# Optimization experiments

Measured on AMD Instinct MI355X. Metric: run time of the kernel, lower is better.

## Reference

```python
import jax, jax.numpy as jnp
import numpy as np

N, D, E = 50000, 128, 800000


def setup_inputs() -> dict:
    key = jax.random.key(0)
    ks = jax.random.split(key, 12)
    s = 1.0 / np.sqrt(D)
    return {
        "x": jax.random.normal(ks[0], (N, D), jnp.float32),
        "edge_index": jax.random.randint(ks[1], (2, E), 0, N, jnp.int32),
        "W1": jax.random.normal(ks[2], (D, D), jnp.float32) * s,
        "bc1": jnp.zeros((D,), jnp.float32),
        "W2": jax.random.normal(ks[3], (D, D), jnp.float32) * s,
        "bc2": jnp.zeros((D,), jnp.float32),
        "w11": jax.random.normal(ks[4], (D, D), jnp.float32) * s,
        "w12": jax.random.normal(ks[5], (D, D), jnp.float32) * s,
        "b1": jax.random.uniform(ks[6], (D,), jnp.float32, -s, s),
        "w21": jax.random.normal(ks[7], (D, D), jnp.float32) * s,
        "w22": jax.random.normal(ks[8], (D, D), jnp.float32) * s,
        "b2": jax.random.uniform(ks[9], (D,), jnp.float32, -s, s),
    }


def gcn_conv(x, W, b, src, dst):
    """PyG GCNConv: self-loops + symmetric D^-1/2 (A+I) D^-1/2 normalization."""
    n = x.shape[0]
    h = x @ W  # [N, D]
    ones = jnp.ones(dst.shape[0], h.dtype)
    deg = jax.ops.segment_sum(ones, dst, num_segments=n) + 1.0  # +1 for self-loop
    dinv = jax.lax.rsqrt(deg)
    norm = dinv[src] * dinv[dst]  # [E]
    agg = jax.ops.segment_sum(h[src] * norm[:, None], dst, num_segments=n)
    agg = agg + h * (dinv * dinv)[:, None]  # self-loop messages
    return agg + b


def reference(x, edge_index, W1, bc1, W2, bc2, w11, w12, b1, w21, w22, b2):
    src, dst = edge_index[0], edge_index[1]
    # layer 1: forward and reversed edge directions (dropout is identity in eval)
    o1 = jax.nn.relu(gcn_conv(x, W1, bc1, src, dst))
    o2 = jax.nn.relu(gcn_conv(x, W1, bc1, dst, src))
    G = jax.nn.sigmoid(o1 @ w11.T + o2 @ w12.T + b1)
    h = G * o1 + (1.0 - G) * o2
    # layer 2
    p1 = jax.nn.relu(gcn_conv(h, W2, bc2, src, dst))
    p2 = jax.nn.relu(gcn_conv(h, W2, bc2, dst, src))
    G2 = jax.nn.sigmoid(p1 @ w21.T + p2 @ w22.T + b2)
    return G2 * p1 + (1.0 - G2) * p2
```

## Files before the change

### kernel.cpp

```cpp
#include <hip/hip_runtime.h>
#include <hip/hip_bf16.h>
#include <hip/hip_fp16.h>
#include <math.h>

#define D 128
#define SEG 4096
#define BSH 7
#define RCAP 4096
#define ACAP 4096

typedef _Float16 half8  __attribute__((ext_vector_type(8)));
typedef _Float16 half4v __attribute__((ext_vector_type(4)));
typedef float    fx4    __attribute__((ext_vector_type(4)));

__global__ __launch_bounds__(256) void scat2_kernel(const int* __restrict__ src,
                                                    const int* __restrict__ dst,
                                                    int e, int nb,
                                                    int* __restrict__ gcur1, int* __restrict__ gcur2,
                                                    unsigned int* __restrict__ rec1,
                                                    unsigned int* __restrict__ rec2) {
    __shared__ int h1[512], h2[512], o1[512], o2[512], run1[512], run2[512];
    int tid = threadIdx.x;
    for (int b = tid; b < nb; b += 256) { h1[b] = 0; h2[b] = 0; run1[b] = 0; run2[b] = 0; }
    __syncthreads();
    int s0 = blockIdx.x * SEG;
    int s1 = min(e, s0 + SEG);
    for (int idx = s0 + tid; idx < s1; idx += 256) {
        atomicAdd(&h1[dst[idx] >> BSH], 1);
        atomicAdd(&h2[src[idx] >> BSH], 1);
    }
    __syncthreads();
    for (int b = tid; b < nb; b += 256) {
        o1[b] = atomicAdd(&gcur1[b], h1[b]);
        o2[b] = atomicAdd(&gcur2[b], h2[b]);
    }
    __syncthreads();
    for (int idx = s0 + tid; idx < s1; idx += 256) {
        unsigned int sv = (unsigned int)src[idx];
        unsigned int dv = (unsigned int)dst[idx];
        int b1 = dv >> BSH, b2 = sv >> BSH;
        int p1 = o1[b1] + atomicAdd(&run1[b1], 1);
        if (p1 < RCAP) rec1[(size_t)b1 * RCAP + p1] = (dv << 16) | sv;
        int p2 = o2[b2] + atomicAdd(&run2[b2], 1);
        if (p2 < RCAP) rec2[(size_t)b2 * RCAP + p2] = (sv << 16) | dv;
    }
}

__global__ __launch_bounds__(256) void fin_kernel(const unsigned int* __restrict__ rec1,
                                                  const unsigned int* __restrict__ rec2,
                                                  const int* __restrict__ gcur1, const int* __restrict__ gcur2,
                                                  unsigned short* __restrict__ adj1, unsigned short* __restrict__ adj2,
                                                  int* __restrict__ ip1, int* __restrict__ ipe1,
                                                  int* __restrict__ ip2, int* __restrict__ ipe2,
                                                  float* __restrict__ dinv1, float* __restrict__ dinv2,
                                                  int n) {
    __shared__ unsigned int Lrec[RCAP];
    __shared__ unsigned short sadj[ACAP];
    __shared__ int deg[128], pscan[128], cur[128];
    __shared__ int ptot_s;
    int bkt = blockIdx.x;
    int dir = blockIdx.y;
    const unsigned int* rec = dir ? rec2 : rec1;
    const int* gc = dir ? gcur2 : gcur1;
    unsigned short* adj = dir ? adj2 : adj1;
    int* ip  = dir ? ip2 : ip1;
    int* ipe = dir ? ipe2 : ipe1;
    float* dinv = dir ? dinv2 : dinv1;

    int tid = threadIdx.x;
    int cnt = gc[bkt];
    if (cnt > RCAP) cnt = RCAP;
    size_t rbase = (size_t)bkt * RCAP;
    if (tid < 128) { deg[tid] = 0; cur[tid] = 0; }
    for (int i = tid; i < cnt; i += 256) Lrec[i] = rec[rbase + i];
    __syncthreads();
    int base = bkt << BSH;
    for (int i = tid; i < cnt; i += 256)
        atomicAdd(&deg[(int)(Lrec[i] >> 16) - base], 1);
    __syncthreads();
    if (tid < 128) pscan[tid] = (deg[tid] + 7) & ~7;
    __syncthreads();
    #pragma unroll
    for (int st = 1; st < 128; st <<= 1) {
        int add = (tid < 128 && tid >= st) ? pscan[tid - st] : 0;
        __syncthreads();
        if (tid < 128) pscan[tid] += add;
        __syncthreads();
    }
    if (tid == 127) ptot_s = min(pscan[127], ACAP);
    __syncthreads();
    int ptot = ptot_s;
    for (int i = tid; i < ptot; i += 256) sadj[i] = (unsigned short)n;
    __syncthreads();
    for (int i = tid; i < cnt; i += 256) {
        unsigned int r = Lrec[i];
        int l = (int)(r >> 16) - base;
        int pd = (deg[l] + 7) & ~7;
        int pos = pscan[l] - pd + atomicAdd(&cur[l], 1);
        if (pos < ACAP) sadj[pos] = (unsigned short)(r & 0xffffu);
    }
    __syncthreads();
    int gbase = bkt * ACAP;
    for (int i = tid; i < ptot; i += 256) adj[gbase + i] = sadj[i];
    if (tid < 128) {
        int node = base + tid;
        if (node < n) {
            int pd = (deg[tid] + 7) & ~7;
            ip[node]  = gbase + pscan[tid] - pd;
            ipe[node] = gbase + pscan[tid];
            dinv[node] = rsqrtf((float)deg[tid] + 1.0f);
        }
    }
    if (bkt == 0 && tid == 200) dinv[n] = 0.0f;
}

__global__ __launch_bounds__(256) void transwh_kernel(const float* __restrict__ W1, const float* __restrict__ W2,
                                                      _Float16* __restrict__ T1, _Float16* __restrict__ T2) {
    __shared__ float s[32][33];
    const float* w = blockIdx.y ? W2 : W1;
    _Float16* t = blockIdx.y ? T2 : T1;
    int tk = (blockIdx.x >> 2) * 32;
    int tc = (blockIdx.x & 3) * 32;
    int lr = threadIdx.x >> 5;
    int lc = threadIdx.x & 31;
    #pragma unroll
    for (int i = 0; i < 32; i += 8)
        s[lr + i][lc] = w[(size_t)(tk + lr + i) * D + tc + lc];
    __syncthreads();
    #pragma unroll
    for (int i = 0; i < 32; i += 8)
        t[(size_t)(tc + lr + i) * D + tk + lc] = (_Float16)s[lc][lr + i];
}

__global__ __launch_bounds__(256) void convh_kernel(const float* __restrict__ w11, const float* __restrict__ w12,
                                                    const float* __restrict__ w21, const float* __restrict__ w22,
                                                    _Float16* __restrict__ o11, _Float16* __restrict__ o12,
                                                    _Float16* __restrict__ o21, _Float16* __restrict__ o22) {
    const float* w = (blockIdx.y == 0) ? w11 : (blockIdx.y == 1) ? w12 : (blockIdx.y == 2) ? w21 : w22;
    _Float16* o = (blockIdx.y == 0) ? o11 : (blockIdx.y == 1) ? o12 : (blockIdx.y == 2) ? o21 : o22;
    int idx = (blockIdx.x * 256 + threadIdx.x) * 4;
    float4 v = *(const float4*)&w[idx];
    half4v h = {(_Float16)v.x, (_Float16)v.y, (_Float16)v.z, (_Float16)v.w};
    *(half4v*)&o[idx] = h;
}

__global__ __launch_bounds__(256) void gemm_f32a_kernel(const float* __restrict__ A,
                                                        const _Float16* __restrict__ Wt,
                                                        _Float16* __restrict__ C16, int n) {
    int tid = threadIdx.x;
    int wv = tid >> 6, lane = tid & 63;
    int m = lane & 15, q = lane >> 4;
    int row0 = blockIdx.x * 128 + wv * 32;
    size_t ar0 = (size_t)min(row0 + m, n - 1) * D;
    size_t ar1 = (size_t)min(row0 + 16 + m, n - 1) * D;
    fx4 acc[2][8];
    #pragma unroll
    for (int t = 0; t < 2; t++)
        #pragma unroll
        for (int ct = 0; ct < 8; ct++) acc[t][ct] = (fx4){0.f, 0.f, 0.f, 0.f};
    #pragma unroll
    for (int ks = 0; ks < 4; ks++) {
        int k0 = ks * 32 + q * 8;
        half8 bf[8];
        #pragma unroll
        for (int ct = 0; ct < 8; ct++)
            bf[ct] = *(const half8*)&Wt[(size_t)(ct * 16 + m) * D + k0];
        float4 u0 = *(const float4*)&A[ar0 + k0];
        float4 u1 = *(const float4*)&A[ar0 + k0 + 4];
        half8 a0 = {(_Float16)u0.x, (_Float16)u0.y, (_Float16)u0.z, (_Float16)u0.w,
                    (_Float16)u1.x, (_Float16)u1.y, (_Float16)u1.z, (_Float16)u1.w};
        float4 v0 = *(const float4*)&A[ar1 + k0];
        float4 v1 = *(const float4*)&A[ar1 + k0 + 4];
        half8 a1 = {(_Float16)v0.x, (_Float16)v0.y, (_Float16)v0.z, (_Float16)v0.w,
                    (_Float16)v1.x, (_Float16)v1.y, (_Float16)v1.z, (_Float16)v1.w};
        #pragma unroll
        for (int ct = 0; ct < 8; ct++) {
            acc[0][ct] = __builtin_amdgcn_mfma_f32_16x16x32_f16(a0, bf[ct], acc[0][ct], 0, 0, 0);
            acc[1][ct] = __builtin_amdgcn_mfma_f32_16x16x32_f16(a1, bf[ct], acc[1][ct], 0, 0, 0);
        }
    }
    #pragma unroll
    for (int t = 0; t < 2; t++)
        #pragma unroll
        for (int reg = 0; reg < 4; reg++) {
            int r = row0 + t * 16 + q * 4 + reg;
            if (r < n) {
                #pragma unroll
                for (int ct = 0; ct < 8; ct++)
                    C16[(size_t)r * D + ct * 16 + m] = (_Float16)acc[t][ct][reg];
            }
        }
}

__global__ __launch_bounds__(256) void gemm_f16a_kernel(const _Float16* __restrict__ A,
                                                        const _Float16* __restrict__ Wt,
                                                        _Float16* __restrict__ C16, int n) {
    int tid = threadIdx.x;
    int wv = tid >> 6, lane = tid & 63;
    int m = lane & 15, q = lane >> 4;
    int row0 = blockIdx.x * 128 + wv * 32;
    size_t ar0 = (size_t)min(row0 + m, n - 1) * D;
    size_t ar1 = (size_t)min(row0 + 16 + m, n - 1) * D;
    fx4 acc[2][8];
    #pragma unroll
    for (int t = 0; t < 2; t++)
        #pragma unroll
        for (int ct = 0; ct < 8; ct++) acc[t][ct] = (fx4){0.f, 0.f, 0.f, 0.f};
    #pragma unroll
    for (int ks = 0; ks < 4; ks++) {
        int k0 = ks * 32 + q * 8;
        half8 bf[8];
        #pragma unroll
        for (int ct = 0; ct < 8; ct++)
            bf[ct] = *(const half8*)&Wt[(size_t)(ct * 16 + m) * D + k0];
        half8 a0 = *(const half8*)&A[ar0 + k0];
        half8 a1 = *(const half8*)&A[ar1 + k0];
        #pragma unroll
        for (int ct = 0; ct < 8; ct++) {
            acc[0][ct] = __builtin_amdgcn_mfma_f32_16x16x32_f16(a0, bf[ct], acc[0][ct], 0, 0, 0);
            acc[1][ct] = __builtin_amdgcn_mfma_f32_16x16x32_f16(a1, bf[ct], acc[1][ct], 0, 0, 0);
        }
    }
    #pragma unroll
    for (int t = 0; t < 2; t++)
        #pragma unroll
        for (int reg = 0; reg < 4; reg++) {
            int r = row0 + t * 16 + q * 4 + reg;
            if (r < n) {
                #pragma unroll
                for (int ct = 0; ct < 8; ct++)
                    C16[(size_t)r * D + ct * 16 + m] = (_Float16)acc[t][ct][reg];
            }
        }
}

__global__ __launch_bounds__(256) void aggregate2_kernel(const __half* __restrict__ h16,
                                                         const int* __restrict__ ip1,
                                                         const int* __restrict__ ipe1,
                                                         const unsigned short* __restrict__ adj1,
                                                         const float* __restrict__ dinv1,
                                                         const int* __restrict__ ip2,
                                                         const int* __restrict__ ipe2,
                                                         const unsigned short* __restrict__ adj2,
                                                         const float* __restrict__ dinv2,
                                                         const float* __restrict__ bias,
                                                         _Float16* __restrict__ out1,
                                                         _Float16* __restrict__ out2, int n) {
    const int* ip  = blockIdx.y ? ip2 : ip1;
    const int* ipe = blockIdx.y ? ipe2 : ipe1;
    const unsigned short* adj = blockIdx.y ? adj2 : adj1;
    const float* dinv = blockIdx.y ? dinv2 : dinv1;
    _Float16* out = blockIdx.y ? out2 : out1;
    int wid = threadIdx.x >> 6, lane = threadIdx.x & 63;
    int half = lane >> 5, l32 = lane & 31;
    int i = blockIdx.x * 4 + wid;
    if (i >= n) return;
    int beg = ip[i], endp = ipe[i];
    int sh = half * 16;
    float4 acc = make_float4(0.f, 0.f, 0.f, 0.f);
    for (int j = beg; j < endp; j += 8) {
        uint4 av = *(const uint4*)&adj[j];
        int s0 = (av.x >> sh) & 0xffff;
        int s1 = (av.y >> sh) & 0xffff;
        int s2 = (av.z >> sh) & 0xffff;
        int s3 = (av.w >> sh) & 0xffff;
        float w0 = dinv[s0], w1 = dinv[s1], w2 = dinv[s2], w3 = dinv[s3];
        uint2 r0 = *(const uint2*)&h16[(size_t)s0 * D + 4 * l32];
        uint2 r1 = *(const uint2*)&h16[(size_t)s1 * D + 4 * l32];
        uint2 r2 = *(const uint2*)&h16[(size_t)s2 * D + 4 * l32];
        uint2 r3 = *(const uint2*)&h16[(size_t)s3 * D + 4 * l32];
        float2 a0 = __half22float2(*(__half2*)&r0.x), b0 = __half22float2(*(__half2*)&r0.y);
        float2 a1 = __half22float2(*(__half2*)&r1.x), b1 = __half22float2(*(__half2*)&r1.y);
        float2 a2 = __half22float2(*(__half2*)&r2.x), b2 = __half22float2(*(__half2*)&r2.y);
        float2 a3 = __half22float2(*(__half2*)&r3.x), b3 = __half22float2(*(__half2*)&r3.y);
        acc.x += w0 * a0.x + w1 * a1.x + w2 * a2.x + w3 * a3.x;
        acc.y += w0 * a0.y + w1 * a1.y + w2 * a2.y + w3 * a3.y;
        acc.z += w0 * b0.x + w1 * b1.x + w2 * b2.x + w3 * b3.x;
        acc.w += w0 * b0.y + w1 * b1.y + w2 * b2.y + w3 * b3.y;
    }
    acc.x += __shfl_xor(acc.x, 32, 64);
    acc.y += __shfl_xor(acc.y, 32, 64);
    acc.z += __shfl_xor(acc.z, 32, 64);
    acc.w += __shfl_xor(acc.w, 32, 64);
    if (half == 0) {
        float di = dinv[i];
        float d2 = di * di;
        uint2 rs = *(const uint2*)&h16[(size_t)i * D + 4 * l32];
        float2 s0 = __half22float2(*(__half2*)&rs.x);
        float2 s1 = __half22float2(*(__half2*)&rs.y);
        float4 bv = *(const float4*)&bias[4 * l32];
        half4v o;
        o[0] = (_Float16)fmaxf(di * acc.x + d2 * s0.x + bv.x, 0.f);
        o[1] = (_Float16)fmaxf(di * acc.y + d2 * s0.y + bv.y, 0.f);
        o[2] = (_Float16)fmaxf(di * acc.z + d2 * s1.x + bv.z, 0.f);
        o[3] = (_Float16)fmaxf(di * acc.w + d2 * s1.y + bv.w, 0.f);
        *(half4v*)&out[(size_t)i * D + 4 * l32] = o;
    }
}

__global__ __launch_bounds__(256) void gate_mfma_kernel(const _Float16* __restrict__ o1,
                                                        const _Float16* __restrict__ o2,
                                                        const _Float16* __restrict__ w1,
                                                        const _Float16* __restrict__ w2,
                                                        const float* __restrict__ b,
                                                        float* __restrict__ out32,
                                                        _Float16* __restrict__ out16,
                                                        int write16, int n) {
    int tid = threadIdx.x;
    int wv = tid >> 6, lane = tid & 63;
    int m = lane & 15, q = lane >> 4;
    int row0 = blockIdx.x * 128 + wv * 32;
    size_t ar0 = (size_t)min(row0 + m, n - 1) * D;
    size_t ar1 = (size_t)min(row0 + 16 + m, n - 1) * D;
    fx4 acc[2][8];
    #pragma unroll
    for (int t = 0; t < 2; t++)
        #pragma unroll
        for (int ct = 0; ct < 8; ct++) acc[t][ct] = (fx4){0.f, 0.f, 0.f, 0.f};
    #pragma unroll
    for (int ks = 0; ks < 4; ks++) {
        int k0 = ks * 32 + q * 8;
        half8 bf1[8], bf2[8];
        #pragma unroll
        for (int ct = 0; ct < 8; ct++) {
            bf1[ct] = *(const half8*)&w1[(size_t)(ct * 16 + m) * D + k0];
            bf2[ct] = *(const half8*)&w2[(size_t)(ct * 16 + m) * D + k0];
        }
        half8 a10 = *(const half8*)&o1[ar0 + k0];
        half8 a20 = *(const half8*)&o2[ar0 + k0];
        half8 a11 = *(const half8*)&o1[ar1 + k0];
        half8 a21 = *(const half8*)&o2[ar1 + k0];
        #pragma unroll
        for (int ct = 0; ct < 8; ct++) {
            acc[0][ct] = __builtin_amdgcn_mfma_f32_16x16x32_f16(a10, bf1[ct], acc[0][ct], 0, 0, 0);
            acc[0][ct] = __builtin_amdgcn_mfma_f32_16x16x32_f16(a20, bf2[ct], acc[0][ct], 0, 0, 0);
            acc[1][ct] = __builtin_amdgcn_mfma_f32_16x16x32_f16(a11, bf1[ct], acc[1][ct], 0, 0, 0);
            acc[1][ct] = __builtin_amdgcn_mfma_f32_16x16x32_f16(a21, bf2[ct], acc[1][ct], 0, 0, 0);
        }
    }
    #pragma unroll
    for (int t = 0; t < 2; t++)
        #pragma unroll
        for (int reg = 0; reg < 4; reg++) {
            int r = row0 + t * 16 + q * 4 + reg;
            if (r < n) {
                #pragma unroll
                for (int ct = 0; ct < 8; ct++) {
                    int c = ct * 16 + m;
                    float tv = acc[t][ct][reg] + b[c];
                    float g = 1.0f / (1.0f + __expf(-tv));
                    float v1 = (float)o1[(size_t)r * D + c];
                    float v2 = (float)o2[(size_t)r * D + c];
                    float res = g * v1 + (1.0f - g) * v2;
                    if (write16) out16[(size_t)r * D + c] = (_Float16)res;
                    else         out32[(size_t)r * D + c] = res;
                }
            }
        }
}

extern "C" void kernel_launch(void* const* d_in, const int* in_sizes, int n_in,
                              void* d_out, int out_size, void* d_ws, size_t ws_size,
                              hipStream_t stream) {
    const float* x   = (const float*)d_in[0];
    const int*   eix = (const int*)d_in[1];
    const float* W1  = (const float*)d_in[2];
    const float* bc1 = (const float*)d_in[3];
    const float* W2  = (const float*)d_in[4];
    const float* bc2 = (const float*)d_in[5];
    const float* w11 = (const float*)d_in[6];
    const float* w12 = (const float*)d_in[7];
    const float* b1  = (const float*)d_in[8];
    const float* w21 = (const float*)d_in[9];
    const float* w22 = (const float*)d_in[10];
    const float* b2  = (const float*)d_in[11];
    int n = in_sizes[0] / D;
    int e = in_sizes[1] / 2;
    const int* src = eix;
    const int* dst = eix + e;

    int nb = (n + 127) >> BSH;
    int nblk = (e + SEG - 1) / SEG;

    char* p = (char*)d_ws;
    auto alloc = [&](size_t bytes) {
        char* q = p;
        p += (bytes + 255) & ~(size_t)255;
        return q;
    };
    int* gcur1 = (int*)alloc((size_t)2 * 512 * sizeof(int));
    int* gcur2 = gcur1 + 512;
    unsigned int* rec1 = (unsigned int*)alloc((size_t)nb * RCAP * sizeof(unsigned int));
    unsigned int* rec2 = (unsigned int*)alloc((size_t)nb * RCAP * sizeof(unsigned int));
    int*   ip1   = (int*)alloc((size_t)n * sizeof(int));
    int*   ipe1  = (int*)alloc((size_t)n * sizeof(int));
    int*   ip2   = (int*)alloc((size_t)n * sizeof(int));
    int*   ipe2  = (int*)alloc((size_t)n * sizeof(int));
    float* dinv1 = (float*)alloc((size_t)(n + 1) * sizeof(float));
    float* dinv2 = (float*)alloc((size_t)(n + 1) * sizeof(float));
    unsigned short* adj1 = (unsigned short*)alloc((size_t)nb * ACAP * sizeof(unsigned short));
    unsigned short* adj2 = (unsigned short*)alloc((size_t)nb * ACAP * sizeof(unsigned short));
    _Float16* W1t  = (_Float16*)alloc((size_t)D * D * sizeof(_Float16));
    _Float16* W2t  = (_Float16*)alloc((size_t)D * D * sizeof(_Float16));
    _Float16* w11h = (_Float16*)alloc((size_t)D * D * sizeof(_Float16));
    _Float16* w12h = (_Float16*)alloc((size_t)D * D * sizeof(_Float16));
    _Float16* w21h = (_Float16*)alloc((size_t)D * D * sizeof(_Float16));
    _Float16* w22h = (_Float16*)alloc((size_t)D * D * sizeof(_Float16));
    _Float16* h16  = (_Float16*)alloc((size_t)(n + 1) * D * sizeof(_Float16));
    _Float16* o1h  = (_Float16*)alloc((size_t)n * D * sizeof(_Float16));
    _Float16* o2h  = (_Float16*)alloc((size_t)n * D * sizeof(_Float16));
    _Float16* h2h  = (_Float16*)alloc((size_t)n * D * sizeof(_Float16));
    float* outF  = (float*)d_out;

    hipMemsetAsync(gcur1, 0, (size_t)2 * 512 * sizeof(int), stream);
    transwh_kernel<<<dim3(16, 2), 256, 0, stream>>>(W1, W2, W1t, W2t);
    convh_kernel<<<dim3(16, 4), 256, 0, stream>>>(w11, w12, w21, w22, w11h, w12h, w21h, w22h);
    scat2_kernel<<<nblk, 256, 0, stream>>>(src, dst, e, nb, gcur1, gcur2, rec1, rec2);
    fin_kernel<<<dim3(nb, 2), 256, 0, stream>>>(rec1, rec2, gcur1, gcur2,
                                                adj1, adj2, ip1, ipe1, ip2, ipe2, dinv1, dinv2, n);

    int gG = (n + 127) / 128;
    int gA = (n + 3) / 4;
    gemm_f32a_kernel<<<gG, 256, 0, stream>>>(x, W1t, h16, n);
    aggregate2_kernel<<<dim3(gA, 2), 256, 0, stream>>>((const __half*)h16,
                                                       ip1, ipe1, adj1, dinv1,
                                                       ip2, ipe2, adj2, dinv2,
                                                       bc1, o1h, o2h, n);
    gate_mfma_kernel<<<gG, 256, 0, stream>>>(o1h, o2h, w11h, w12h, b1,
                                             nullptr, h2h, 1, n);
    gemm_f16a_kernel<<<gG, 256, 0, stream>>>(h2h, W2t, h16, n);
    aggregate2_kernel<<<dim3(gA, 2), 256, 0, stream>>>((const __half*)h16,
                                                       ip1, ipe1, adj1, dinv1,
                                                       ip2, ipe2, adj2, dinv2,
                                                       bc2, o1h, o2h, n);
    gate_mfma_kernel<<<gG, 256, 0, stream>>>(o1h, o2h, w21h, w22h, b2,
                                             outF, nullptr, 0, n);
}
```

Measured before the change: 355.9 us.

## Split aggregation into feature chunks with 8 neighbors per wave, merge prep kernels

The aggregation kernel is restructured so each block of 512 threads handles 8 nodes for one 32-feature chunk. Each wave processes 16 neighbors per iteration, with 8 lanes per neighbor reading 8-byte feature slices, and the results are reduced with shuffles. Adjacency padding grows from 8 to 16 to match the new stride. Nodes in a block group are interleaved across chunks so that feature rows may be reused in cache. The two weight-prep kernels are merged into one launch. The risks are more wasted padding slots per node, four times as many passes over the index lists, and narrower per-lane loads.

```diff
diff --git a/kernel.cpp b/kernel.cpp
--- a/kernel.cpp
+++ b/kernel.cpp
@@ -78,7 +78,7 @@
     for (int i = tid; i < cnt; i += 256)
         atomicAdd(&deg[(int)(Lrec[i] >> 16) - base], 1);
     __syncthreads();
-    if (tid < 128) pscan[tid] = (deg[tid] + 7) & ~7;
+    if (tid < 128) pscan[tid] = (deg[tid] + 15) & ~15;
     __syncthreads();
     #pragma unroll
     for (int st = 1; st < 128; st <<= 1) {
@@ -95,7 +95,7 @@
     for (int i = tid; i < cnt; i += 256) {
         unsigned int r = Lrec[i];
         int l = (int)(r >> 16) - base;
-        int pd = (deg[l] + 7) & ~7;
+        int pd = (deg[l] + 15) & ~15;
         int pos = pscan[l] - pd + atomicAdd(&cur[l], 1);
         if (pos < ACAP) sadj[pos] = (unsigned short)(r & 0xffffu);
     }
@@ -105,7 +105,7 @@
     if (tid < 128) {
         int node = base + tid;
         if (node < n) {
-            int pd = (deg[tid] + 7) & ~7;
+            int pd = (deg[tid] + 15) & ~15;
             ip[node]  = gbase + pscan[tid] - pd;
             ipe[node] = gbase + pscan[tid];
             dinv[node] = rsqrtf((float)deg[tid] + 1.0f);
@@ -114,34 +114,37 @@
     if (bkt == 0 && tid == 200) dinv[n] = 0.0f;
 }
 
-__global__ __launch_bounds__(256) void transwh_kernel(const float* __restrict__ W1, const float* __restrict__ W2,
-                                                      _Float16* __restrict__ T1, _Float16* __restrict__ T2) {
+__global__ __launch_bounds__(256) void prep_kernel(const float* __restrict__ W1, const float* __restrict__ W2,
+                                                   const float* __restrict__ w11, const float* __restrict__ w12,
+                                                   const float* __restrict__ w21, const float* __restrict__ w22,
+                                                   _Float16* __restrict__ T1, _Float16* __restrict__ T2,
+                                                   _Float16* __restrict__ o11, _Float16* __restrict__ o12,
+                                                   _Float16* __restrict__ o21, _Float16* __restrict__ o22) {
     __shared__ float s[32][33];
-    const float* w = blockIdx.y ? W2 : W1;
-    _Float16* t = blockIdx.y ? T2 : T1;
-    int tk = (blockIdx.x >> 2) * 32;
-    int tc = (blockIdx.x & 3) * 32;
-    int lr = threadIdx.x >> 5;
-    int lc = threadIdx.x & 31;
-    #pragma unroll
-    for (int i = 0; i < 32; i += 8)
-        s[lr + i][lc] = w[(size_t)(tk + lr + i) * D + tc + lc];
-    __syncthreads();
-    #pragma unroll
-    for (int i = 0; i < 32; i += 8)
-        t[(size_t)(tc + lr + i) * D + tk + lc] = (_Float16)s[lc][lr + i];
-}
-
-__global__ __launch_bounds__(256) void convh_kernel(const float* __restrict__ w11, const float* __restrict__ w12,
-                                                    const float* __restrict__ w21, const float* __restrict__ w22,
-                                                    _Float16* __restrict__ o11, _Float16* __restrict__ o12,
-                                                    _Float16* __restrict__ o21, _Float16* __restrict__ o22) {
-    const float* w = (blockIdx.y == 0) ? w11 : (blockIdx.y == 1) ? w12 : (blockIdx.y == 2) ? w21 : w22;
-    _Float16* o = (blockIdx.y == 0) ? o11 : (blockIdx.y == 1) ? o12 : (blockIdx.y == 2) ? o21 : o22;
-    int idx = (blockIdx.x * 256 + threadIdx.x) * 4;
-    float4 v = *(const float4*)&w[idx];
-    half4v h = {(_Float16)v.x, (_Float16)v.y, (_Float16)v.z, (_Float16)v.w};
-    *(half4v*)&o[idx] = h;
+    int which = blockIdx.y;
+    if (which < 2) {
+        const float* w = which ? W2 : W1;
+        _Float16* t = which ? T2 : T1;
+        int tk = (blockIdx.x >> 2) * 32;
+        int tc = (blockIdx.x & 3) * 32;
+        int lr = threadIdx.x >> 5;
+        int lc = threadIdx.x & 31;
+        #pragma unroll
+        for (int i = 0; i < 32; i += 8)
+            s[lr + i][lc] = w[(size_t)(tk + lr + i) * D + tc + lc];
+        __syncthreads();
+        #pragma unroll
+        for (int i = 0; i < 32; i += 8)
+            t[(size_t)(tc + lr + i) * D + tk + lc] = (_Float16)s[lc][lr + i];
+    } else {
+        int wsel = which - 2;
+        const float* w = (wsel == 0) ? w11 : (wsel == 1) ? w12 : (wsel == 2) ? w21 : w22;
+        _Float16* o = (wsel == 0) ? o11 : (wsel == 1) ? o12 : (wsel == 2) ? o21 : o22;
+        int idx = (blockIdx.x * 256 + threadIdx.x) * 4;
+        float4 v = *(const float4*)&w[idx];
+        half4v h = {(_Float16)v.x, (_Float16)v.y, (_Float16)v.z, (_Float16)v.w};
+        *(half4v*)&o[idx] = h;
+    }
 }
 
 __global__ __launch_bounds__(256) void gemm_f32a_kernel(const float* __restrict__ A,
@@ -234,7 +237,7 @@
         }
 }
 
-__global__ __launch_bounds__(256) void aggregate2_kernel(const __half* __restrict__ h16,
+__global__ __launch_bounds__(512) void aggregate4_kernel(const __half* __restrict__ h16,
                                                          const int* __restrict__ ip1,
                                                          const int* __restrict__ ipe1,
                                                          const unsigned short* __restrict__ adj1,
@@ -251,50 +254,50 @@
     const unsigned short* adj = blockIdx.y ? adj2 : adj1;
     const float* dinv = blockIdx.y ? dinv2 : dinv1;
     _Float16* out = blockIdx.y ? out2 : out1;
+    int b = blockIdx.x;
+    int chunk = (b & 7) >> 1;
+    int pp = b & 1;
+    int g = b >> 3;
     int wid = threadIdx.x >> 6, lane = threadIdx.x & 63;
-    int half = lane >> 5, l32 = lane & 31;
-    int i = blockIdx.x * 4 + wid;
-    if (i >= n) return;
-    int beg = ip[i], endp = ipe[i];
-    int sh = half * 16;
+    int node = (g * 2 + pp) * 8 + wid;
+    if (node >= n) return;
+    int ns = lane >> 3;
+    int fo = chunk * 32 + ((lane & 7) << 2);
+    int beg = ip[node], endp = ipe[node];
     float4 acc = make_float4(0.f, 0.f, 0.f, 0.f);
-    for (int j = beg; j < endp; j += 8) {
-        uint4 av = *(const uint4*)&adj[j];
-        int s0 = (av.x >> sh) & 0xffff;
-        int s1 = (av.y >> sh) & 0xffff;
-        int s2 = (av.z >> sh) & 0xffff;
-        int s3 = (av.w >> sh) & 0xffff;
-        float w0 = dinv[s0], w1 = dinv[s1], w2 = dinv[s2], w3 = dinv[s3];
-        uint2 r0 = *(const uint2*)&h16[(size_t)s0 * D + 4 * l32];
-        uint2 r1 = *(const uint2*)&h16[(size_t)s1 * D + 4 * l32];
-        uint2 r2 = *(const uint2*)&h16[(size_t)s2 * D + 4 * l32];
-        uint2 r3 = *(const uint2*)&h16[(size_t)s3 * D + 4 * l32];
-        float2 a0 = __half22float2(*(__half2*)&r0.x), b0 = __half22float2(*(__half2*)&r0.y);
-        float2 a1 = __half22float2(*(__half2*)&r1.x), b1 = __half22float2(*(__half2*)&r1.y);
-        float2 a2 = __half22float2(*(__half2*)&r2.x), b2 = __half22float2(*(__half2*)&r2.y);
-        float2 a3 = __half22float2(*(__half2*)&r3.x), b3 = __half22float2(*(__half2*)&r3.y);
-        acc.x += w0 * a0.x + w1 * a1.x + w2 * a2.x + w3 * a3.x;
-        acc.y += w0 * a0.y + w1 * a1.y + w2 * a2.y + w3 * a3.y;
-        acc.z += w0 * b0.x + w1 * b1.x + w2 * b2.x + w3 * b3.x;
-        acc.w += w0 * b0.y + w1 * b1.y + w2 * b2.y + w3 * b3.y;
-    }
-    acc.x += __shfl_xor(acc.x, 32, 64);
-    acc.y += __shfl_xor(acc.y, 32, 64);
-    acc.z += __shfl_xor(acc.z, 32, 64);
-    acc.w += __shfl_xor(acc.w, 32, 64);
-    if (half == 0) {
-        float di = dinv[i];
+    for (int j = beg; j < endp; j += 16) {
+        int sA = adj[j + ns];
+        int sB = adj[j + 8 + ns];
+        float wA = dinv[sA], wB = dinv[sB];
+        uint2 rA = *(const uint2*)&h16[(size_t)sA * D + fo];
+        uint2 rB = *(const uint2*)&h16[(size_t)sB * D + fo];
+        float2 a0 = __half22float2(*(__half2*)&rA.x), a1 = __half22float2(*(__half2*)&rA.y);
+        float2 b0 = __half22float2(*(__half2*)&rB.x), b1 = __half22float2(*(__half2*)&rB.y);
+        acc.x += wA * a0.x + wB * b0.x;
+        acc.y += wA * a0.y + wB * b0.y;
+        acc.z += wA * a1.x + wB * b1.x;
+        acc.w += wA * a1.y + wB * b1.y;
+    }
+    #pragma unroll
+    for (int off = 8; off < 64; off <<= 1) {
+        acc.x += __shfl_xor(acc.x, off, 64);
+        acc.y += __shfl_xor(acc.y, off, 64);
+        acc.z += __shfl_xor(acc.z, off, 64);
+        acc.w += __shfl_xor(acc.w, off, 64);
+    }
+    if (lane < 8) {
+        float di = dinv[node];
         float d2 = di * di;
-        uint2 rs = *(const uint2*)&h16[(size_t)i * D + 4 * l32];
+        uint2 rs = *(const uint2*)&h16[(size_t)node * D + fo];
         float2 s0 = __half22float2(*(__half2*)&rs.x);
         float2 s1 = __half22float2(*(__half2*)&rs.y);
-        float4 bv = *(const float4*)&bias[4 * l32];
+        float4 bv = *(const float4*)&bias[fo];
         half4v o;
         o[0] = (_Float16)fmaxf(di * acc.x + d2 * s0.x + bv.x, 0.f);
         o[1] = (_Float16)fmaxf(di * acc.y + d2 * s0.y + bv.y, 0.f);
         o[2] = (_Float16)fmaxf(di * acc.z + d2 * s1.x + bv.z, 0.f);
         o[3] = (_Float16)fmaxf(di * acc.w + d2 * s1.y + bv.w, 0.f);
-        *(half4v*)&out[(size_t)i * D + 4 * l32] = o;
+        *(half4v*)&out[(size_t)node * D + fo] = o;
     }
 }
 
@@ -413,23 +416,23 @@
     float* outF  = (float*)d_out;
 
     hipMemsetAsync(gcur1, 0, (size_t)2 * 512 * sizeof(int), stream);
-    transwh_kernel<<<dim3(16, 2), 256, 0, stream>>>(W1, W2, W1t, W2t);
-    convh_kernel<<<dim3(16, 4), 256, 0, stream>>>(w11, w12, w21, w22, w11h, w12h, w21h, w22h);
+    prep_kernel<<<dim3(16, 6), 256, 0, stream>>>(W1, W2, w11, w12, w21, w22,
+                                                 W1t, W2t, w11h, w12h, w21h, w22h);
     scat2_kernel<<<nblk, 256, 0, stream>>>(src, dst, e, nb, gcur1, gcur2, rec1, rec2);
     fin_kernel<<<dim3(nb, 2), 256, 0, stream>>>(rec1, rec2, gcur1, gcur2,
                                                 adj1, adj2, ip1, ipe1, ip2, ipe2, dinv1, dinv2, n);
 
     int gG = (n + 127) / 128;
-    int gA = (n + 3) / 4;
+    int gA = 8 * ((n + 15) / 16);
     gemm_f32a_kernel<<<gG, 256, 0, stream>>>(x, W1t, h16, n);
-    aggregate2_kernel<<<dim3(gA, 2), 256, 0, stream>>>((const __half*)h16,
+    aggregate4_kernel<<<dim3(gA, 2), 512, 0, stream>>>((const __half*)h16,
                                                        ip1, ipe1, adj1, dinv1,
                                                        ip2, ipe2, adj2, dinv2,
                                                        bc1, o1h, o2h, n);
     gate_mfma_kernel<<<gG, 256, 0, stream>>>(o1h, o2h, w11h, w12h, b1,
                                              nullptr, h2h, 1, n);
     gemm_f16a_kernel<<<gG, 256, 0, stream>>>(h2h, W2t, h16, n);
-    aggregate2_kernel<<<dim3(gA, 2), 256, 0, stream>>>((const __half*)h16,
+    aggregate4_kernel<<<dim3(gA, 2), 512, 0, stream>>>((const __half*)h16,
                                                        ip1, ipe1, adj1, dinv1,
                                                        ip2, ipe2, adj2, dinv2,
                                                        bc2, o1h, o2h, n);
```

Measured after the change: 532.4 us. 1.5x slower.
